# Optimization experiments

Hardware: AMD Instinct MI355X
Metric: run time of the kernel (lower is better)

The kernel has to match this reference:

```python
import jax, jax.numpy as jnp
import numpy as np

B, CIN, COUT, H, W = 4, 256, 256, 96, 96
GN_GROUPS = 16
EPS = 1e-5


def setup_inputs() -> dict:
    key = jax.random.key(0)
    k0, k1, k2, k3 = jax.random.split(key, 4)
    x = jax.random.normal(k0, (B, CIN, H, W), jnp.float32)
    offset = jax.random.normal(k1, (B, 18, H, W), jnp.float32)
    mask = jax.random.uniform(k2, (B, 9, H, W), jnp.float32)  # modulation scalars (sigmoid-range)
    weight = jax.random.normal(k3, (COUT, CIN, 3, 3), jnp.float32) * 0.02
    gamma = jnp.ones((COUT,), jnp.float32)
    beta = jnp.zeros((COUT,), jnp.float32)
    return {"x": x, "offset": offset, "mask": mask, "weight": weight, "gamma": gamma, "beta": beta}


def _bilinear(xf, py, px, Hs, Ws):
    # xf: [B, C, H*W] flattened input; py/px: [B, H, W] sample coords -> [B, C, H, W]
    y0 = jnp.floor(py)
    x0 = jnp.floor(px)
    acc = jnp.zeros((xf.shape[0], xf.shape[1], py.shape[1], py.shape[2]), xf.dtype)
    for dy in (0, 1):
        for dx in (0, 1):
            yy = y0 + dy
            xx = x0 + dx
            wgt = (1.0 - jnp.abs(py - yy)) * (1.0 - jnp.abs(px - xx))
            valid = (yy >= 0) & (yy < Hs) & (xx >= 0) & (xx < Ws)  # zero-pad outside
            yi = jnp.clip(yy, 0, Hs - 1).astype(jnp.int32)
            xi = jnp.clip(xx, 0, Ws - 1).astype(jnp.int32)
            idx = (yi * Ws + xi).reshape(py.shape[0], -1)  # [B, H*W]
            g = jax.vmap(lambda xb, ib: xb[:, ib])(xf, idx)  # [B, C, H*W]
            g = g.reshape(acc.shape)
            acc = acc + g * (wgt * valid.astype(xf.dtype))[:, None]
    return acc


def _modulated_deform_conv(x, offset, mask, weight):
    # 3x3, stride=1, pad=1, dilation=1, deform_groups=1, no bias
    Bz, C, Hs, Ws = x.shape
    hh = jnp.arange(Hs, dtype=x.dtype)
    ww = jnp.arange(Ws, dtype=x.dtype)
    base_y, base_x = jnp.meshgrid(hh, ww, indexing="ij")  # [H, W]
    xf = x.reshape(Bz, C, Hs * Ws)
    out = jnp.zeros((Bz, weight.shape[0], Hs, Ws), x.dtype)
    for k in range(9):  # fixed 3x3 kernel taps
        ki, kj = k // 3, k % 3
        py = base_y[None] + (ki - 1) + offset[:, 2 * k]      # dy channel
        px = base_x[None] + (kj - 1) + offset[:, 2 * k + 1]  # dx channel
        val = _bilinear(xf, py, px, Hs, Ws) * mask[:, k][:, None]  # [B, CIN, H, W]
        out = out + jnp.einsum("oc,bchw->bohw", weight[:, :, ki, kj], val)
    return out


def _group_norm(x, gamma, beta):
    Bz, C, Hs, Ws = x.shape
    xr = x.reshape(Bz, GN_GROUPS, C // GN_GROUPS, Hs, Ws)
    mu = xr.mean(axis=(2, 3, 4), keepdims=True)
    var = xr.var(axis=(2, 3, 4), keepdims=True)
    xn = ((xr - mu) * jax.lax.rsqrt(var + EPS)).reshape(Bz, C, Hs, Ws)
    return xn * gamma[None, :, None, None] + beta[None, :, None, None]


def reference(x, offset, mask, weight, gamma, beta):
    y = _modulated_deform_conv(x, offset, mask, weight)
    return _group_norm(y, gamma, beta)
```

## Files before the change

kernel.cpp:

```cpp
#include <hip/hip_runtime.h>
#include <hip/hip_bf16.h>
#include <cstdint>

typedef short  short8  __attribute__((ext_vector_type(8)));
typedef ushort ushort8 __attribute__((ext_vector_type(8)));
typedef float  f32x4   __attribute__((ext_vector_type(4)));

#define BATCH 4
#define CIN   256
#define COUT  256
#define HH    96
#define WW    96
#define HWSZ  9216
#define GN_G  16
#define EPSV  1e-5f
#define BN    144
#define NPB   64
#define NWG   (BATCH*NPB)

__device__ __forceinline__ float bf2f(ushort u) {
    return __uint_as_float(((uint32_t)u) << 16);
}
__device__ __forceinline__ ushort f2bf(float f) {
    uint32_t u = __float_as_uint(f);
    u += 0x7FFFu + ((u >> 16) & 1u);
    return (ushort)(u >> 16);
}

__global__ __launch_bounds__(256)
void nhwc_kernel(const float* __restrict__ x, ushort* __restrict__ xn) {
    __shared__ ushort tile[64][66];
    const int b  = blockIdx.z;
    const int cb = blockIdx.y * 64;
    const int pb = blockIdx.x * 64;
    const int t  = threadIdx.x;
    {
        const int pl = t & 63;
        const int cq = t >> 6;
        #pragma unroll
        for (int i = 0; i < 16; ++i) {
            const int c = cq * 16 + i;
            tile[c][pl] = f2bf(x[((size_t)b * CIN + cb + c) * HWSZ + pb + pl]);
        }
    }
    __syncthreads();
    {
        const int cl = t & 63;
        const int pq = t >> 6;
        #pragma unroll
        for (int i = 0; i < 16; ++i) {
            const int p = pq * 16 + i;
            xn[((size_t)b * HWSZ + pb + p) * CIN + cb + cl] = tile[cl][p];
        }
    }
}

__global__ __launch_bounds__(256)
void repack_w_kernel(const float* __restrict__ w, ushort* __restrict__ wp) {
    const int d    = blockIdx.x * 256 + threadIdx.x;
    const int j    = d & 7;
    const int cout = (d >> 3) & 255;
    const int kb8  = d >> 11;
    const int ktap = kb8 >> 5;
    const int cin  = ((kb8 & 31) << 3) | j;
    wp[d] = f2bf(w[cout * (CIN * 9) + cin * 9 + ktap]);
}

__global__ __launch_bounds__(512, 2)
void dcn_mfma_kernel(const ushort* __restrict__ xn, const float* __restrict__ off,
                     const float* __restrict__ msk, const ushort* __restrict__ wp,
                     float* __restrict__ out, float* __restrict__ part) {
    __shared__ ushort buf[2][BN * 128];
    __shared__ int    s_idx[2][BN][4];
    __shared__ float  s_wgt[2][BN][4];

    const int bid  = blockIdx.x;
    const int swz  = (bid & 7) * (NWG / 8) + (bid >> 3);
    const int b    = swz / NPB;
    const int pblk = swz - b * NPB;
    const int p0   = pblk * BN;

    const int t    = threadIdx.x;
    const int lane = t & 63;
    const int wid  = t >> 6;

    auto coords = [&](int k) {
        if (t < BN) {
            const int slot = k & 1;
            const int pos  = p0 + t;
            const int hh   = pos / WW;
            const int ww   = pos - hh * WW;
            const size_t obase = ((size_t)b * 18 + 2 * k) * HWSZ + pos;
            const float oy = off[obase];
            const float ox = off[obase + HWSZ];
            const float m  = msk[((size_t)b * 9 + k) * HWSZ + pos];
            const float py = (float)(hh + k / 3 - 1) + oy;
            const float px = (float)(ww + k % 3 - 1) + ox;
            const float y0 = floorf(py), x0 = floorf(px);
            #pragma unroll
            for (int dy = 0; dy < 2; ++dy)
                #pragma unroll
                for (int dx = 0; dx < 2; ++dx) {
                    const float yy = y0 + (float)dy, xx = x0 + (float)dx;
                    const float wb = (1.f - fabsf(py - yy)) * (1.f - fabsf(px - xx));
                    const bool valid = (yy >= 0.f) && (yy < (float)HH) && (xx >= 0.f) && (xx < (float)WW);
                    int yi = (int)yy; yi = yi < 0 ? 0 : (yi > HH - 1 ? HH - 1 : yi);
                    int xi = (int)xx; xi = xi < 0 ? 0 : (xi > WW - 1 ? WW - 1 : xi);
                    s_idx[slot][t][dy * 2 + dx] = yi * WW + xi;
                    s_wgt[slot][t][dy * 2 + dx] = valid ? wb * m : 0.f;
                }
        }
    };

    const int sp  = lane >> 4;
    const int c16 = lane & 15;
    auto stage = [&](int c, ushort* dstbuf) {
        const int tap  = c >> 1;
        const int half = c & 1;
        const int slot = tap & 1;
        const ushort* xb = xn + (size_t)b * HWSZ * CIN + half * 128 + c16 * 8;
        #pragma unroll
        for (int g = 0; g < 5; ++g) {
            const bool active = (g < 4) || (sp < 2);
            const int p = wid * 18 + ((g < 4) ? (g * 4 + sp) : (16 + sp));
            if (active) {
                float vacc[8] = {0.f, 0.f, 0.f, 0.f, 0.f, 0.f, 0.f, 0.f};
                #pragma unroll
                for (int cr = 0; cr < 4; ++cr) {
                    const int   ix = s_idx[slot][p][cr];
                    const float w  = s_wgt[slot][p][cr];
                    const ushort8 v = *(const ushort8*)(xb + (size_t)ix * CIN);
                    #pragma unroll
                    for (int j = 0; j < 8; ++j)
                        vacc[j] += w * bf2f(v[j]);
                }
                ushort8 o;
                #pragma unroll
                for (int j = 0; j < 8; j += 2) {
                    const __hip_bfloat162 h2 = __float22bfloat162_rn(float2{vacc[j], vacc[j + 1]});
                    const uint32_t u = *reinterpret_cast<const uint32_t*>(&h2);
                    o[j]     = (ushort)u;
                    o[j + 1] = (ushort)(u >> 16);
                }
                char* drow = (char*)dstbuf + p * 256;
                *(ushort8*)(drow + ((c16 * 16) ^ ((p & 15) << 4))) = o;
            }
        }
    };

    f32x4 acc[2][9];
    #pragma unroll
    for (int i = 0; i < 2; ++i)
        #pragma unroll
        for (int j = 0; j < 9; ++j)
            acc[i][j] = (f32x4){0.f, 0.f, 0.f, 0.f};

    const int arow = lane & 15;
    const int akb  = lane >> 4;
    const int asw  = arow << 4;

    auto loadA = [&](int kb8base, int ks, short8 af[2]) {
        const ushort* wrow = wp + ((size_t)(kb8base + ks * 4 + akb) * COUT + wid * 32 + arow) * 8;
        #pragma unroll
        for (int mt = 0; mt < 2; ++mt)
            af[mt] = *(const short8*)(wrow + mt * 16 * 8);
    };

    auto mfma_chunk = [&](int kb8base, const ushort* src, short8 afA[2]) {
        const char* srow = (const char*)src;
        short8 afB[2];
        #pragma unroll
        for (int ks = 0; ks < 4; ++ks) {
            if (ks < 3) loadA(kb8base, ks + 1, (ks & 1) ? afA : afB);
            short8* afc = (ks & 1) ? afB : afA;
            const int cb = (ks * 64 + akb * 16) ^ asw;
            #pragma unroll
            for (int nt = 0; nt < 9; ++nt) {
                const int row = arow + nt * 16;
                const short8 bfr = *(const short8*)(srow + row * 256 + ((ks * 64 + akb * 16) ^ ((row & 15) << 4)));
                #pragma unroll
                for (int mt = 0; mt < 2; ++mt)
                    acc[mt][nt] = __builtin_amdgcn_mfma_f32_16x16x32_bf16(
                        afc[mt], bfr, acc[mt][nt], 0, 0, 0);
            }
            (void)cb;
        }
    };

    coords(0);
    __syncthreads();
    stage(0, buf[0]);
    __syncthreads();
    for (int c = 0; c < 18; ++c) {
        if (c < 17) stage(c + 1, buf[(c + 1) & 1]);
        if (!(c & 1) && (c >> 1) + 1 < 9) coords((c >> 1) + 1);
        short8 afA[2];
        loadA(c * 16, 0, afA);
        mfma_chunk(c * 16, buf[c & 1], afA);
        __syncthreads();
    }

    const int prow = lane & 15;
    const int crow = (lane >> 4) * 4;
    #pragma unroll
    for (int mt = 0; mt < 2; ++mt) {
        const int cout = wid * 32 + mt * 16 + crow;
        #pragma unroll
        for (int nt = 0; nt < 9; ++nt) {
            const int opos = p0 + nt * 16 + prow;
            float* op = out + ((size_t)b * COUT + cout) * HWSZ + opos;
            #pragma unroll
            for (int r = 0; r < 4; ++r)
                op[(size_t)r * HWSZ] = acc[mt][nt][r];
        }
    }

    #pragma unroll
    for (int mt = 0; mt < 2; ++mt) {
        float s = 0.f, q = 0.f;
        #pragma unroll
        for (int nt = 0; nt < 9; ++nt)
            #pragma unroll
            for (int r = 0; r < 4; ++r) {
                const float v = acc[mt][nt][r];
                s += v; q += v * v;
            }
        #pragma unroll
        for (int o = 32; o > 0; o >>= 1) {
            s += __shfl_xor(s, o);
            q += __shfl_xor(q, o);
        }
        if (lane == 0) {
            const int bg = b * GN_G + wid * 2 + mt;
            part[((size_t)bg * NPB + pblk) * 2]     = s;
            part[((size_t)bg * NPB + pblk) * 2 + 1] = q;
        }
    }
}

__global__ void gn_final_kernel(const float* __restrict__ part, float* __restrict__ stats) {
    const int t  = threadIdx.x;
    const int bg = t >> 2;
    const int j  = t & 3;
    float s = 0.f, q = 0.f;
    for (int i = j; i < NPB; i += 4) {
        s += part[((size_t)bg * NPB + i) * 2];
        q += part[((size_t)bg * NPB + i) * 2 + 1];
    }
    s += __shfl_xor(s, 1); q += __shfl_xor(q, 1);
    s += __shfl_xor(s, 2); q += __shfl_xor(q, 2);
    if (j == 0) {
        const float invn = 1.f / (float)((COUT / GN_G) * HWSZ);
        const float mean = s * invn;
        stats[bg * 2]     = mean;
        stats[bg * 2 + 1] = q * invn - mean * mean;
    }
}

__global__ __launch_bounds__(256)
void gn_apply_kernel(float* __restrict__ y, const float* __restrict__ stats,
                     const float* __restrict__ gamma, const float* __restrict__ beta) {
    const int i = blockIdx.x * 256 + threadIdx.x;
    const int e = i * 4;
    const int c  = (e / HWSZ) & (COUT - 1);
    const int bg = e / (HWSZ * (COUT / GN_G));
    const float mean = stats[bg * 2];
    const float var  = stats[bg * 2 + 1];
    const float inv  = rsqrtf(var + EPSV);
    const float sc = inv * gamma[c];
    const float sh = beta[c] - mean * sc;
    float4 v = ((float4*)y)[i];
    v.x = v.x * sc + sh;
    v.y = v.y * sc + sh;
    v.z = v.z * sc + sh;
    v.w = v.w * sc + sh;
    ((float4*)y)[i] = v;
}

extern "C" void kernel_launch(void* const* d_in, const int* in_sizes, int n_in,
                              void* d_out, int out_size, void* d_ws, size_t ws_size,
                              hipStream_t stream) {
    const float* x      = (const float*)d_in[0];
    const float* offset = (const float*)d_in[1];
    const float* mask   = (const float*)d_in[2];
    const float* weight = (const float*)d_in[3];
    const float* gamma  = (const float*)d_in[4];
    const float* beta   = (const float*)d_in[5];
    float* out = (float*)d_out;

    ushort* xn    = (ushort*)d_ws;
    ushort* wp    = xn + (size_t)BATCH * HWSZ * CIN;
    float*  part  = (float*)(wp + (size_t)9 * CIN * COUT);
    float*  stats = part + (size_t)BATCH * GN_G * NPB * 2;

    {
        dim3 g(HWSZ / 64, CIN / 64, BATCH);
        nhwc_kernel<<<g, 256, 0, stream>>>(x, xn);
    }
    repack_w_kernel<<<9 * CIN * COUT / 256, 256, 0, stream>>>(weight, wp);

    dcn_mfma_kernel<<<NWG, 512, 0, stream>>>(xn, offset, mask, wp, out, part);

    gn_final_kernel<<<1, 256, 0, stream>>>(part, stats);
    gn_apply_kernel<<<(size_t)BATCH * COUT * HWSZ / 4 / 256, 256, 0, stream>>>(out, stats, gamma, beta);
}
```

Measured before the change: 110.3 us.

## Fuse GroupNorm into deform-conv kernel via cooperative grid sync

Turns the MFMA deform-conv kernel into a cooperative launch. Each block writes its partial statistics, waits at a grid-wide barrier, reduces the per-group mean and variance itself, and applies the normalisation to its accumulators in registers before the single output store. This drops the separate stats and apply kernels and the extra read and write of the fp32 output. In exchange, all 256 blocks of 512 threads must be co-resident, the barrier adds a sync cost, and the accumulators stay live across the barrier.

```diff
diff --git a/kernel.cpp b/kernel.cpp
--- a/kernel.cpp
+++ b/kernel.cpp
@@ -1,6 +1,9 @@
 #include <hip/hip_runtime.h>
 #include <hip/hip_bf16.h>
+#include <hip/hip_cooperative_groups.h>
 #include <cstdint>
+
+namespace cg = cooperative_groups;
 
 typedef short  short8  __attribute__((ext_vector_type(8)));
 typedef ushort ushort8 __attribute__((ext_vector_type(8)));
@@ -69,10 +72,12 @@
 __global__ __launch_bounds__(512, 2)
 void dcn_mfma_kernel(const ushort* __restrict__ xn, const float* __restrict__ off,
                      const float* __restrict__ msk, const ushort* __restrict__ wp,
+                     const float* __restrict__ gamma, const float* __restrict__ beta,
                      float* __restrict__ out, float* __restrict__ part) {
     __shared__ ushort buf[2][BN * 128];
     __shared__ int    s_idx[2][BN][4];
     __shared__ float  s_wgt[2][BN][4];
+    __shared__ float  s_stats[GN_G][2];
 
     const int bid  = blockIdx.x;
     const int swz  = (bid & 7) * (NWG / 8) + (bid >> 3);
@@ -157,7 +162,6 @@
 
     const int arow = lane & 15;
     const int akb  = lane >> 4;
-    const int asw  = arow << 4;
 
     auto loadA = [&](int kb8base, int ks, short8 af[2]) {
         const ushort* wrow = wp + ((size_t)(kb8base + ks * 4 + akb) * COUT + wid * 32 + arow) * 8;
@@ -173,7 +177,6 @@
         for (int ks = 0; ks < 4; ++ks) {
             if (ks < 3) loadA(kb8base, ks + 1, (ks & 1) ? afA : afB);
             short8* afc = (ks & 1) ? afB : afA;
-            const int cb = (ks * 64 + akb * 16) ^ asw;
             #pragma unroll
             for (int nt = 0; nt < 9; ++nt) {
                 const int row = arow + nt * 16;
@@ -183,7 +186,6 @@
                     acc[mt][nt] = __builtin_amdgcn_mfma_f32_16x16x32_bf16(
                         afc[mt], bfr, acc[mt][nt], 0, 0, 0);
             }
-            (void)cb;
         }
     };
 
@@ -200,81 +202,73 @@
         __syncthreads();
     }
 
+    #pragma unroll
+    for (int mt = 0; mt < 2; ++mt) {
+        float s = 0.f, q = 0.f;
+        #pragma unroll
+        for (int nt = 0; nt < 9; ++nt)
+            #pragma unroll
+            for (int r = 0; r < 4; ++r) {
+                const float v = acc[mt][nt][r];
+                s += v; q += v * v;
+            }
+        #pragma unroll
+        for (int o = 32; o > 0; o >>= 1) {
+            s += __shfl_xor(s, o);
+            q += __shfl_xor(q, o);
+        }
+        if (lane == 0) {
+            const int bg = b * GN_G + wid * 2 + mt;
+            part[((size_t)bg * NPB + pblk) * 2]     = s;
+            part[((size_t)bg * NPB + pblk) * 2 + 1] = q;
+        }
+    }
+
+    __threadfence();
+    cg::this_grid().sync();
+
+    for (int g = wid; g < GN_G; g += 8) {
+        const float* pg = part + ((size_t)(b * GN_G + g) * NPB + lane) * 2;
+        float s = pg[0];
+        float q = pg[1];
+        #pragma unroll
+        for (int o = 32; o > 0; o >>= 1) {
+            s += __shfl_xor(s, o);
+            q += __shfl_xor(q, o);
+        }
+        if (lane == 0) {
+            const float invn = 1.f / (float)((COUT / GN_G) * HWSZ);
+            const float mean = s * invn;
+            const float var  = q * invn - mean * mean;
+            s_stats[g][0] = mean;
+            s_stats[g][1] = rsqrtf(var + EPSV);
+        }
+    }
+    __syncthreads();
+
     const int prow = lane & 15;
     const int crow = (lane >> 4) * 4;
     #pragma unroll
     for (int mt = 0; mt < 2; ++mt) {
         const int cout = wid * 32 + mt * 16 + crow;
+        const int g    = wid * 2 + mt;
+        const float mean = s_stats[g][0];
+        const float inv  = s_stats[g][1];
+        float sc[4], sh[4];
+        #pragma unroll
+        for (int r = 0; r < 4; ++r) {
+            sc[r] = inv * gamma[cout + r];
+            sh[r] = beta[cout + r] - mean * sc[r];
+        }
         #pragma unroll
         for (int nt = 0; nt < 9; ++nt) {
             const int opos = p0 + nt * 16 + prow;
             float* op = out + ((size_t)b * COUT + cout) * HWSZ + opos;
             #pragma unroll
             for (int r = 0; r < 4; ++r)
-                op[(size_t)r * HWSZ] = acc[mt][nt][r];
-        }
-    }
-
-    #pragma unroll
-    for (int mt = 0; mt < 2; ++mt) {
-        float s = 0.f, q = 0.f;
-        #pragma unroll
-        for (int nt = 0; nt < 9; ++nt)
-            #pragma unroll
-            for (int r = 0; r < 4; ++r) {
-                const float v = acc[mt][nt][r];
-                s += v; q += v * v;
-            }
-        #pragma unroll
-        for (int o = 32; o > 0; o >>= 1) {
-            s += __shfl_xor(s, o);
-            q += __shfl_xor(q, o);
-        }
-        if (lane == 0) {
-            const int bg = b * GN_G + wid * 2 + mt;
-            part[((size_t)bg * NPB + pblk) * 2]     = s;
-            part[((size_t)bg * NPB + pblk) * 2 + 1] = q;
-        }
-    }
-}
-
-__global__ void gn_final_kernel(const float* __restrict__ part, float* __restrict__ stats) {
-    const int t  = threadIdx.x;
-    const int bg = t >> 2;
-    const int j  = t & 3;
-    float s = 0.f, q = 0.f;
-    for (int i = j; i < NPB; i += 4) {
-        s += part[((size_t)bg * NPB + i) * 2];
-        q += part[((size_t)bg * NPB + i) * 2 + 1];
-    }
-    s += __shfl_xor(s, 1); q += __shfl_xor(q, 1);
-    s += __shfl_xor(s, 2); q += __shfl_xor(q, 2);
-    if (j == 0) {
-        const float invn = 1.f / (float)((COUT / GN_G) * HWSZ);
-        const float mean = s * invn;
-        stats[bg * 2]     = mean;
-        stats[bg * 2 + 1] = q * invn - mean * mean;
-    }
-}
-
-__global__ __launch_bounds__(256)
-void gn_apply_kernel(float* __restrict__ y, const float* __restrict__ stats,
-                     const float* __restrict__ gamma, const float* __restrict__ beta) {
-    const int i = blockIdx.x * 256 + threadIdx.x;
-    const int e = i * 4;
-    const int c  = (e / HWSZ) & (COUT - 1);
-    const int bg = e / (HWSZ * (COUT / GN_G));
-    const float mean = stats[bg * 2];
-    const float var  = stats[bg * 2 + 1];
-    const float inv  = rsqrtf(var + EPSV);
-    const float sc = inv * gamma[c];
-    const float sh = beta[c] - mean * sc;
-    float4 v = ((float4*)y)[i];
-    v.x = v.x * sc + sh;
-    v.y = v.y * sc + sh;
-    v.z = v.z * sc + sh;
-    v.w = v.w * sc + sh;
-    ((float4*)y)[i] = v;
+                op[(size_t)r * HWSZ] = acc[mt][nt][r] * sc[r] + sh[r];
+        }
+    }
 }
 
 extern "C" void kernel_launch(void* const* d_in, const int* in_sizes, int n_in,
@@ -288,10 +282,9 @@
     const float* beta   = (const float*)d_in[5];
     float* out = (float*)d_out;
 
-    ushort* xn    = (ushort*)d_ws;
-    ushort* wp    = xn + (size_t)BATCH * HWSZ * CIN;
-    float*  part  = (float*)(wp + (size_t)9 * CIN * COUT);
-    float*  stats = part + (size_t)BATCH * GN_G * NPB * 2;
+    ushort* xn   = (ushort*)d_ws;
+    ushort* wp   = xn + (size_t)BATCH * HWSZ * CIN;
+    float*  part = (float*)(wp + (size_t)9 * CIN * COUT);
 
     {
         dim3 g(HWSZ / 64, CIN / 64, BATCH);
@@ -299,8 +292,8 @@
     }
     repack_w_kernel<<<9 * CIN * COUT / 256, 256, 0, stream>>>(weight, wp);
 
-    dcn_mfma_kernel<<<NWG, 512, 0, stream>>>(xn, offset, mask, wp, out, part);
-
-    gn_final_kernel<<<1, 256, 0, stream>>>(part, stats);
-    gn_apply_kernel<<<(size_t)BATCH * COUT * HWSZ / 4 / 256, 256, 0, stream>>>(out, stats, gamma, beta);
-}
+    void* args[] = {(void*)&xn, (void*)&offset, (void*)&mask, (void*)&wp,
+                    (void*)&gamma, (void*)&beta, (void*)&out, (void*)&part};
+    hipLaunchCooperativeKernel((void*)dcn_mfma_kernel, dim3(NWG), dim3(512),
+                               args, 0, stream);
+}
```

Measured after the change: 157.7 us. +42.9%, slower.

## Split K across wave pairs with wider cout tiles and an LDS reduction

Applied to the files above, without the earlier changes.

The 8 waves are regrouped into 4 output-channel groups of 64 channels times 2 K-halves. Each wave now computes a 4x9 MFMA tile over half of each 64-wide K chunk, which halves the shared-memory B-fragment reads per wave at the same MFMA count. The two K-halves are then summed through LDS before the output stores and the GroupNorm partial statistics. In exchange the accumulator register footprint doubles, which risks spills under launch_bounds(512,2), and the reduction adds extra barriers and LDS traffic.

```diff
diff --git a/kernel.cpp b/kernel.cpp
--- a/kernel.cpp
+++ b/kernel.cpp
@@ -70,7 +70,7 @@
 void dcn_mfma_kernel(const ushort* __restrict__ xn, const float* __restrict__ off,
                      const float* __restrict__ msk, const ushort* __restrict__ wp,
                      float* __restrict__ out, float* __restrict__ part) {
-    __shared__ ushort buf[2][BN * 128];
+    __shared__ __align__(16) ushort buf[2][BN * 128];
     __shared__ int    s_idx[2][BN][4];
     __shared__ float  s_wgt[2][BN][4];
 
@@ -83,6 +83,8 @@
     const int t    = threadIdx.x;
     const int lane = t & 63;
     const int wid  = t >> 6;
+    const int cg   = wid & 3;
+    const int kh   = wid >> 2;
 
     auto coords = [&](int k) {
         if (t < BN) {
@@ -148,42 +150,40 @@
         }
     };
 
-    f32x4 acc[2][9];
+    f32x4 acc[4][9];
     #pragma unroll
-    for (int i = 0; i < 2; ++i)
+    for (int i = 0; i < 4; ++i)
         #pragma unroll
         for (int j = 0; j < 9; ++j)
             acc[i][j] = (f32x4){0.f, 0.f, 0.f, 0.f};
 
     const int arow = lane & 15;
     const int akb  = lane >> 4;
-    const int asw  = arow << 4;
-
-    auto loadA = [&](int kb8base, int ks, short8 af[2]) {
-        const ushort* wrow = wp + ((size_t)(kb8base + ks * 4 + akb) * COUT + wid * 32 + arow) * 8;
-        #pragma unroll
-        for (int mt = 0; mt < 2; ++mt)
+
+    auto loadA = [&](int kb8base, int ks, short8 af[4]) {
+        const ushort* wrow = wp + ((size_t)(kb8base + ks * 4 + akb) * COUT + cg * 64 + arow) * 8;
+        #pragma unroll
+        for (int mt = 0; mt < 4; ++mt)
             af[mt] = *(const short8*)(wrow + mt * 16 * 8);
     };
 
-    auto mfma_chunk = [&](int kb8base, const ushort* src, short8 afA[2]) {
+    auto mfma_chunk = [&](int kb8base, const ushort* src, short8 afA[4]) {
         const char* srow = (const char*)src;
-        short8 afB[2];
-        #pragma unroll
-        for (int ks = 0; ks < 4; ++ks) {
-            if (ks < 3) loadA(kb8base, ks + 1, (ks & 1) ? afA : afB);
-            short8* afc = (ks & 1) ? afB : afA;
-            const int cb = (ks * 64 + akb * 16) ^ asw;
+        short8 afB[4];
+        #pragma unroll
+        for (int ks = 0; ks < 2; ++ks) {
+            const int ksg = kh * 2 + ks;
+            if (ks == 0) loadA(kb8base, kh * 2 + 1, afB);
+            short8* afc = ks ? afB : afA;
             #pragma unroll
             for (int nt = 0; nt < 9; ++nt) {
                 const int row = arow + nt * 16;
-                const short8 bfr = *(const short8*)(srow + row * 256 + ((ks * 64 + akb * 16) ^ ((row & 15) << 4)));
-                #pragma unroll
-                for (int mt = 0; mt < 2; ++mt)
+                const short8 bfr = *(const short8*)(srow + row * 256 + ((ksg * 64 + akb * 16) ^ ((row & 15) << 4)));
+                #pragma unroll
+                for (int mt = 0; mt < 4; ++mt)
                     acc[mt][nt] = __builtin_amdgcn_mfma_f32_16x16x32_bf16(
                         afc[mt], bfr, acc[mt][nt], 0, 0, 0);
             }
-            (void)cb;
         }
     };
 
@@ -194,46 +194,68 @@
     for (int c = 0; c < 18; ++c) {
         if (c < 17) stage(c + 1, buf[(c + 1) & 1]);
         if (!(c & 1) && (c >> 1) + 1 < 9) coords((c >> 1) + 1);
-        short8 afA[2];
-        loadA(c * 16, 0, afA);
+        short8 afA[4];
+        loadA(c * 16, kh * 2, afA);
         mfma_chunk(c * 16, buf[c & 1], afA);
         __syncthreads();
     }
 
-    const int prow = lane & 15;
-    const int crow = (lane >> 4) * 4;
-    #pragma unroll
-    for (int mt = 0; mt < 2; ++mt) {
-        const int cout = wid * 32 + mt * 16 + crow;
-        #pragma unroll
-        for (int nt = 0; nt < 9; ++nt) {
-            const int opos = p0 + nt * 16 + prow;
-            float* op = out + ((size_t)b * COUT + cout) * HWSZ + opos;
-            #pragma unroll
-            for (int r = 0; r < 4; ++r)
-                op[(size_t)r * HWSZ] = acc[mt][nt][r];
-        }
-    }
-
-    #pragma unroll
-    for (int mt = 0; mt < 2; ++mt) {
-        float s = 0.f, q = 0.f;
-        #pragma unroll
-        for (int nt = 0; nt < 9; ++nt)
-            #pragma unroll
-            for (int r = 0; r < 4; ++r) {
-                const float v = acc[mt][nt][r];
-                s += v; q += v * v;
-            }
-        #pragma unroll
-        for (int o = 32; o > 0; o >>= 1) {
-            s += __shfl_xor(s, o);
-            q += __shfl_xor(q, o);
-        }
-        if (lane == 0) {
-            const int bg = b * GN_G + wid * 2 + mt;
-            part[((size_t)bg * NPB + pblk) * 2]     = s;
-            part[((size_t)bg * NPB + pblk) * 2 + 1] = q;
+    {
+        f32x4* s_xch = reinterpret_cast<f32x4*>(&buf[0][0]);
+        const int plane = cg * 64 + lane;
+        #pragma unroll
+        for (int mt = 0; mt < 4; ++mt) {
+            if (wid >= 4) {
+                #pragma unroll
+                for (int nt = 0; nt < 9; ++nt)
+                    s_xch[plane * 10 + nt] = acc[mt][nt];
+            }
+            __syncthreads();
+            if (wid < 4) {
+                #pragma unroll
+                for (int nt = 0; nt < 9; ++nt)
+                    acc[mt][nt] += s_xch[plane * 10 + nt];
+            }
+            __syncthreads();
+        }
+    }
+
+    if (wid < 4) {
+        const int prow = lane & 15;
+        const int crow = (lane >> 4) * 4;
+        #pragma unroll
+        for (int mt = 0; mt < 4; ++mt) {
+            const int cout = cg * 64 + mt * 16 + crow;
+            #pragma unroll
+            for (int nt = 0; nt < 9; ++nt) {
+                const int opos = p0 + nt * 16 + prow;
+                float* op = out + ((size_t)b * COUT + cout) * HWSZ + opos;
+                #pragma unroll
+                for (int r = 0; r < 4; ++r)
+                    op[(size_t)r * HWSZ] = acc[mt][nt][r];
+            }
+        }
+
+        #pragma unroll
+        for (int mt = 0; mt < 4; ++mt) {
+            float s = 0.f, q = 0.f;
+            #pragma unroll
+            for (int nt = 0; nt < 9; ++nt)
+                #pragma unroll
+                for (int r = 0; r < 4; ++r) {
+                    const float v = acc[mt][nt][r];
+                    s += v; q += v * v;
+                }
+            #pragma unroll
+            for (int o = 32; o > 0; o >>= 1) {
+                s += __shfl_xor(s, o);
+                q += __shfl_xor(q, o);
+            }
+            if (lane == 0) {
+                const int bg = b * GN_G + cg * 4 + mt;
+                part[((size_t)bg * NPB + pblk) * 2]     = s;
+                part[((size_t)bg * NPB + pblk) * 2 + 1] = q;
+            }
         }
     }
 }
```

Result: faster. 105.0 us (-4.9%).
